# Optimization experiments

Hardware: AMD Instinct MI355X
Metric: run time of the kernel (lower is better)

The kernel has to match this reference:

```python
import jax, jax.numpy as jnp
import numpy as np

N, E, IN, H, C, ED = 100000, 1600000, 128, 4, 32, 16
HC = H * C
NEG_SLOPE = 0.2
EPS = 1e-5


def setup_inputs() -> dict:
    key = jax.random.key(0)
    ks = jax.random.split(key, 12)
    x = jax.random.normal(ks[0], (N, IN), jnp.float32)
    edge_index = jax.random.randint(ks[1], (2, E), 0, N, dtype=jnp.int32)
    edge_attr = jax.random.normal(ks[2], (E, ED), jnp.float32)
    s_in = 1.0 / np.sqrt(IN)
    s_ed = 1.0 / np.sqrt(ED)
    s_c = 1.0 / np.sqrt(C)
    Wl = jax.random.normal(ks[3], (IN, HC), jnp.float32) * s_in
    bl = jnp.zeros((HC,), jnp.float32)
    Wr = jax.random.normal(ks[4], (IN, HC), jnp.float32) * s_in
    br = jnp.zeros((HC,), jnp.float32)
    We = jax.random.normal(ks[5], (ED, HC), jnp.float32) * s_ed
    att = jax.random.normal(ks[6], (H, C), jnp.float32) * s_c
    bias = jnp.zeros((HC,), jnp.float32)
    ln_weight = jnp.ones((HC,), jnp.float32)
    ln_bias = jnp.zeros((HC,), jnp.float32)
    return {"x": x, "edge_index": edge_index, "edge_attr": edge_attr,
            "Wl": Wl, "bl": bl, "Wr": Wr, "br": br, "We": We,
            "att": att, "bias": bias, "ln_weight": ln_weight, "ln_bias": ln_bias}


def gatv2_block(x, src, dst, edge_attr, Wl, bl, Wr, br, We, att, bias, ln_weight, ln_bias):
    n = x.shape[0]
    xl = (x @ Wl + bl).reshape(n, H, C)  # source-side transform
    xr = (x @ Wr + br).reshape(n, H, C)  # target-side transform
    # add_self_loops with fill_value='mean': self-loop edge_attr = mean of
    # incoming edge_attr per node (0 for isolated nodes)
    ea_sum = jax.ops.segment_sum(edge_attr, dst, num_segments=n)
    cnt = jax.ops.segment_sum(jnp.ones((edge_attr.shape[0],), edge_attr.dtype), dst, num_segments=n)
    self_attr = ea_sum / jnp.maximum(cnt, 1.0)[:, None]
    loop = jnp.arange(n, dtype=src.dtype)
    src_a = jnp.concatenate([src, loop])
    dst_a = jnp.concatenate([dst, loop])
    ea_a = jnp.concatenate([edge_attr, self_attr], axis=0)
    e_emb = (ea_a @ We).reshape(-1, H, C)
    # GATv2 attention: a^T LeakyReLU(xl_j + xr_i + e)
    m = xl[src_a] + xr[dst_a] + e_emb            # [Etot, H, C]
    m = jax.nn.leaky_relu(m, NEG_SLOPE)
    alpha = jnp.einsum('ehc,hc->eh', m, att)     # [Etot, H]
    amax = jax.ops.segment_max(alpha, dst_a, num_segments=n)
    alpha = jnp.exp(alpha - amax[dst_a])
    denom = jax.ops.segment_sum(alpha, dst_a, num_segments=n)
    alpha = alpha / denom[dst_a]
    out = jax.ops.segment_sum(xl[src_a] * alpha[:, :, None], dst_a, num_segments=n)
    h = out.reshape(n, HC) + bias
    # residual (in_dim == H*C so no projection), PyG graph-mode LayerNorm
    z = x + h
    mu = jnp.mean(z)
    var = jnp.mean((z - mu) ** 2)
    z = (z - mu) / jnp.sqrt(var + EPS)
    z = z * ln_weight + ln_bias
    return jax.nn.relu(z)  # dropout = identity in eval


def reference(x, edge_index, edge_attr, Wl, bl, Wr, br, We, att, bias, ln_weight, ln_bias):
    src, dst = edge_index[0], edge_index[1]
    return gatv2_block(x, src, dst, edge_attr, Wl, bl, Wr, br, We, att, bias, ln_weight, ln_bias)
```

## Files before the change

kernel.cpp:

```cpp
#include <hip/hip_runtime.h>
#include <hip/hip_bf16.h>

static constexpr float NEG_SLOPE = 0.2f;
static constexpr float LN_EPS = 1e-5f;

typedef float v2f __attribute__((ext_vector_type(2)));
typedef __attribute__((ext_vector_type(8))) short bf16x8;
typedef __attribute__((ext_vector_type(4))) float f32x4;

__device__ __forceinline__ unsigned f2b(float f) {
  unsigned u = __float_as_uint(f);
  return (u + 0x7fffu + ((u >> 16) & 1u)) >> 16;
}
__device__ __forceinline__ v2f b2f2(ushort2 u) {
  v2f r;
  r.x = __uint_as_float((unsigned)u.x << 16);
  r.y = __uint_as_float((unsigned)u.y << 16);
  return r;
}
__device__ __forceinline__ float sbl(unsigned w) {
  return __uint_as_float(w << 16);
}
__device__ __forceinline__ float sbh(unsigned w) {
  return __uint_as_float(w & 0xFFFF0000u);
}

__device__ __forceinline__ float head_sum16(float x) {
  float t;
  t = __int_as_float(__builtin_amdgcn_update_dpp(
      0, __float_as_int(x), 0xB1, 0xF, 0xF, true));
  x += t;
  t = __int_as_float(__builtin_amdgcn_update_dpp(
      0, __float_as_int(x), 0x4E, 0xF, 0xF, true));
  x += t;
  t = __int_as_float(__builtin_amdgcn_update_dpp(
      0, __float_as_int(x), 0x124, 0xF, 0xF, true));
  x += t;
  t = __int_as_float(__builtin_amdgcn_update_dpp(
      0, __float_as_int(x), 0x128, 0xF, 0xF, true));
  x += t;
  return x;
}

__global__ __launch_bounds__(256) void k_packB(
    const float* __restrict__ Wl, const float* __restrict__ Wr,
    const float* __restrict__ bl, const float* __restrict__ br,
    ushort* __restrict__ Bpack, float* __restrict__ bcat,
    int* __restrict__ degcur, int N2, int* __restrict__ tot,
    int* __restrict__ src_pad, double* __restrict__ red)
{
  int tid = blockIdx.x * 256 + threadIdx.x;
  int l = tid & 63, s = (tid >> 6) & 3, t = tid >> 8;
  int col = t * 16 + (l & 15);
  int kb = s * 32 + (l >> 4) * 8;
  const float* __restrict__ W = (col < 128) ? Wl : Wr;
  int c = col & 127;
  unsigned p[4];
#pragma unroll
  for (int i = 0; i < 4; ++i) {
    unsigned lo = f2b(W[(size_t)(kb + 2 * i) * 128 + c]);
    unsigned hi = f2b(W[(size_t)(kb + 2 * i + 1) * 128 + c]);
    p[i] = lo | (hi << 16);
  }
  *(uint4*)(Bpack + (size_t)tid * 8) = make_uint4(p[0], p[1], p[2], p[3]);
  if (tid < 256) bcat[tid] = (tid < 128) ? bl[tid] : br[tid - 128];
  if (tid < 8) src_pad[tid] = 0;
  if (tid < 2) red[tid] = 0.0;
  if (tid == 0) *tot = 0;
  for (int i = tid; i < N2; i += 4096) degcur[i] = 0;
}

__global__ __launch_bounds__(256) void k_gemm_mfma(
    const float* __restrict__ x, const ushort* __restrict__ Bpack,
    const float* __restrict__ bcat, ushort* __restrict__ xl,
    float* __restrict__ outz, int n, const int* __restrict__ dst,
    int* __restrict__ deg, int E)
{
  const int lane = threadIdx.x & 63;
  const int w = threadIdx.x >> 6;
  const int row0 = blockIdx.x * 64 + w * 16;
  const int rowA = min(row0 + (lane & 15), n - 1);
  const int kgrp = lane >> 4;

  f32x4 acc[16];
#pragma unroll
  for (int t = 0; t < 16; ++t) acc[t] = (f32x4){0.f, 0.f, 0.f, 0.f};

#pragma unroll
  for (int s = 0; s < 4; ++s) {
    const float4* ap =
        (const float4*)(x + (size_t)rowA * 128 + s * 32 + kgrp * 8);
    float4 a0 = ap[0], a1 = ap[1];
    bf16x8 a;
    a[0] = (short)f2b(a0.x); a[1] = (short)f2b(a0.y);
    a[2] = (short)f2b(a0.z); a[3] = (short)f2b(a0.w);
    a[4] = (short)f2b(a1.x); a[5] = (short)f2b(a1.y);
    a[6] = (short)f2b(a1.z); a[7] = (short)f2b(a1.w);
#pragma unroll
    for (int t = 0; t < 16; ++t) {
      bf16x8 b =
          *(const bf16x8*)(Bpack + (((size_t)t * 4 + s) * 64 + lane) * 8);
      acc[t] = __builtin_amdgcn_mfma_f32_16x16x32_bf16(a, b, acc[t], 0, 0, 0);
    }
  }

  const int colg = lane & 15;
  const int rbase = row0 + (lane >> 4) * 4;
#pragma unroll
  for (int t = 0; t < 16; ++t) {
    const int col = t * 16 + colg;
    const float bia = bcat[col];
    if (col < 128) {
#pragma unroll
      for (int r = 0; r < 4; ++r) {
        const int R = rbase + r;
        if (R < n) xl[(size_t)R * 128 + col] = (ushort)f2b(acc[t][r] + bia);
      }
    } else {
      const int c = col - 128;
#pragma unroll
      for (int r = 0; r < 4; ++r) {
        const int R = rbase + r;
        if (R < n) outz[(size_t)R * 128 + c] = acc[t][r] + bia;
      }
    }
  }

  for (int e = blockIdx.x * 256 + threadIdx.x; e < E; e += gridDim.x * 256)
    atomicAdd(&deg[dst[e]], 1);
}

__global__ __launch_bounds__(256) void k_allocscan(
    const int* __restrict__ deg, int* __restrict__ offs, int* __restrict__ tot,
    int n)
{
  __shared__ int s[256];
  __shared__ int base;
  const int b = blockIdx.x, t = threadIdx.x, i = b * 256 + t;
  const int v = (i < n) ? deg[i] : 0;
  s[t] = v;
  __syncthreads();
  for (int o = 1; o < 256; o <<= 1) {
    int u = (t >= o) ? s[t - o] : 0;
    __syncthreads();
    s[t] += u;
    __syncthreads();
  }
  if (t == 255) base = atomicAdd(tot, s[255]);
  __syncthreads();
  if (i < n) offs[i] = base + s[t] - v;
}

__global__ __launch_bounds__(256) void k_fill(
    const int* __restrict__ src, const int* __restrict__ dst,
    const int* __restrict__ offs, int* __restrict__ cursor,
    const float4* __restrict__ ea4, int* __restrict__ csr_src,
    ushort* __restrict__ csr_ea, int E)
{
  int e = blockIdx.x * 256 + threadIdx.x;
  if (e >= E) return;
  int d = dst[e];
  int pos = offs[d] + atomicAdd(&cursor[d], 1);
  csr_src[pos] = src[e];
  float4 r0 = ea4[(size_t)e * 4 + 0], r1 = ea4[(size_t)e * 4 + 1];
  float4 r2 = ea4[(size_t)e * 4 + 2], r3 = ea4[(size_t)e * 4 + 3];
  uint4* o4 = (uint4*)(csr_ea + (size_t)pos * 16);
  o4[0] = make_uint4(f2b(r0.x) | (f2b(r0.y) << 16), f2b(r0.z) | (f2b(r0.w) << 16),
                     f2b(r1.x) | (f2b(r1.y) << 16), f2b(r1.z) | (f2b(r1.w) << 16));
  o4[1] = make_uint4(f2b(r2.x) | (f2b(r2.y) << 16), f2b(r2.z) | (f2b(r2.w) << 16),
                     f2b(r3.x) | (f2b(r3.y) << 16), f2b(r3.z) | (f2b(r3.w) << 16));
}

__global__ __launch_bounds__(256) void k_fused(
    const int* __restrict__ csr_src, const ushort* __restrict__ csr_ea,
    const int* __restrict__ offs, const int* __restrict__ deg,
    const ushort* __restrict__ xl, const float* __restrict__ We,
    const float* __restrict__ att, const float* __restrict__ x,
    const float* __restrict__ bias, float* __restrict__ outz,
    double* __restrict__ red, int N)
{
  const int lane = threadIdx.x & 63;
  const int gw =
      __builtin_amdgcn_readfirstlane(blockIdx.x * 4 + (threadIdx.x >> 6));
  const int nw = gridDim.x * 4;
  const v2f* __restrict__ We2 = (const v2f*)We;
  const v2f* __restrict__ X2 = (const v2f*)x;
  v2f* __restrict__ Z2 = (v2f*)outz;

  v2f we[16];
#pragma unroll
  for (int k = 0; k < 16; ++k) we[k] = We2[k * 64 + lane];
  const v2f a2 = ((const v2f*)att)[lane];
  const v2f b2 = ((const v2f*)bias)[lane];

  float sred = 0.f, s2red = 0.f;

  for (int node = gw; node < N; node += nw) {
    const int beg = offs[node];
    const int len = deg[node];
    const v2f xrv = Z2[(size_t)node * 64 + lane];
    const v2f xvSelf =
        b2f2(*(const ushort2*)(xl + (size_t)node * 128 + 2 * lane));

    float dA = 0.f, dB = 0.f;
    v2f aA = {0.f, 0.f}, aB = {0.f, 0.f};
    v2f embsum = {0.f, 0.f};

    auto edgeU = [&](v2f xv, uint4 lo, uint4 hi, float& den, v2f& acc) {
      v2f emb = sbl(lo.x) * we[0];
      emb += sbh(lo.x) * we[1];
      emb += sbl(lo.y) * we[2];
      emb += sbh(lo.y) * we[3];
      emb += sbl(lo.z) * we[4];
      emb += sbh(lo.z) * we[5];
      emb += sbl(lo.w) * we[6];
      emb += sbh(lo.w) * we[7];
      emb += sbl(hi.x) * we[8];
      emb += sbh(hi.x) * we[9];
      emb += sbl(hi.y) * we[10];
      emb += sbh(hi.y) * we[11];
      emb += sbl(hi.z) * we[12];
      emb += sbh(hi.z) * we[13];
      emb += sbl(hi.w) * we[14];
      emb += sbh(hi.w) * we[15];
      embsum += emb;
      v2f mm = xv + xrv + emb;
      v2f ml;
      ml.x = fmaxf(mm.x, NEG_SLOPE * mm.x);
      ml.y = fmaxf(mm.y, NEG_SLOPE * mm.y);
      const float part = head_sum16(fmaf(ml.y, a2.y, ml.x * a2.x));
      const float p = __expf(part);
      den += p;
      acc += xv * p;
    };

    const int nB = len >> 1;
    const int nA = len - nB;
    const int bB = beg + nA;

    uint4 eAlo = {0, 0, 0, 0}, eAhi = {0, 0, 0, 0};
    uint4 eBlo = {0, 0, 0, 0}, eBhi = {0, 0, 0, 0};
    v2f xvA = {0.f, 0.f}, xvB = {0.f, 0.f};
    int sA1 = 0, sB1 = 0;

    if (len > 0) {
      const uint4* pa = (const uint4*)(csr_ea + (size_t)beg * 16);
      eAlo = pa[0];
      eAhi = pa[1];
      const int sA0 = csr_src[beg];
      xvA = b2f2(*(const ushort2*)(xl + (size_t)sA0 * 128 + 2 * lane));
      sA1 = csr_src[beg + 1];
    }
    if (nB > 0) {
      const uint4* pb = (const uint4*)(csr_ea + (size_t)bB * 16);
      eBlo = pb[0];
      eBhi = pb[1];
      const int sB0 = csr_src[bB];
      xvB = b2f2(*(const ushort2*)(xl + (size_t)sB0 * 128 + 2 * lane));
      sB1 = csr_src[bB + 1];
    }

    for (int i = 0; i < nB; ++i) {
      const uint4* pa = (const uint4*)(csr_ea + (size_t)(beg + i + 1) * 16);
      const uint4* pb = (const uint4*)(csr_ea + (size_t)(bB + i + 1) * 16);
      const uint4 nAlo = pa[0], nAhi = pa[1];
      const uint4 nBlo = pb[0], nBhi = pb[1];
      const v2f xvA1 =
          b2f2(*(const ushort2*)(xl + (size_t)sA1 * 128 + 2 * lane));
      const v2f xvB1 =
          b2f2(*(const ushort2*)(xl + (size_t)sB1 * 128 + 2 * lane));
      const int sA2 = csr_src[beg + i + 2];
      const int sB2 = csr_src[bB + i + 2];
      edgeU(xvA, eAlo, eAhi, dA, aA);
      edgeU(xvB, eBlo, eBhi, dB, aB);
      eAlo = nAlo; eAhi = nAhi; eBlo = nBlo; eBhi = nBhi;
      xvA = xvA1; xvB = xvB1;
      sA1 = sA2; sB1 = sB2;
    }
    if (nA > nB) {
      edgeU(xvA, eAlo, eAhi, dA, aA);
    }

    {
      const float inv = (len > 0) ? 1.f / (float)len : 0.f;
      const v2f embS = embsum * inv;
      v2f mm = xvSelf + xrv + embS;
      v2f ml;
      ml.x = fmaxf(mm.x, NEG_SLOPE * mm.x);
      ml.y = fmaxf(mm.y, NEG_SLOPE * mm.y);
      const float part = head_sum16(fmaf(ml.y, a2.y, ml.x * a2.x));
      const float p = __expf(part);
      dA += p;
      aA += xvSelf * p;
    }

    const float den = dA + dB;
    const float invden = 1.f / den;
    const float o0 = (aA.x + aB.x) * invden;
    const float o1 = (aA.y + aB.y) * invden;

    const v2f xvn = X2[(size_t)node * 64 + lane];
    const float v0 = xvn.x + o0 + b2.x;
    const float v1 = xvn.y + o1 + b2.y;
    Z2[(size_t)node * 64 + lane] = (v2f){v0, v1};
    sred += v0 + v1;
    s2red += v0 * v0 + v1 * v1;
  }

#pragma unroll
  for (int o = 32; o > 0; o >>= 1) {
    sred += __shfl_down(sred, o);
    s2red += __shfl_down(s2red, o);
  }
  __shared__ double ls[4], ls2[4];
  const int w = threadIdx.x >> 6;
  if ((threadIdx.x & 63) == 0) {
    ls[w] = (double)sred;
    ls2[w] = (double)s2red;
  }
  __syncthreads();
  if (threadIdx.x == 0) {
    unsafeAtomicAdd(red, ls[0] + ls[1] + ls[2] + ls[3]);
    unsafeAtomicAdd(red + 1, ls2[0] + ls2[1] + ls2[2] + ls2[3]);
  }
}

__global__ __launch_bounds__(256) void k_final(
    float* __restrict__ z, const double* __restrict__ red,
    const float* __restrict__ lnw, const float* __restrict__ lnb, int M4)
{
  int i = blockIdx.x * 256 + threadIdx.x;
  if (i >= M4) return;
  const double invM = 1.0 / ((double)M4 * 4.0);
  const double mu = red[0] * invM;
  const double var = red[1] * invM - mu * mu;
  const float sc = rsqrtf((float)var + LN_EPS);
  const float muf = (float)mu;
  const float4* W4 = (const float4*)lnw;
  const float4* L4 = (const float4*)lnb;
  float4* Z4 = (float4*)z;
  float4 zv = Z4[i], wv = W4[i & 31], lv = L4[i & 31];
  float4 o;
  o.x = fmaxf((zv.x - muf) * sc * wv.x + lv.x, 0.f);
  o.y = fmaxf((zv.y - muf) * sc * wv.y + lv.y, 0.f);
  o.z = fmaxf((zv.z - muf) * sc * wv.z + lv.z, 0.f);
  o.w = fmaxf((zv.w - muf) * sc * wv.w + lv.w, 0.f);
  Z4[i] = o;
}

extern "C" void kernel_launch(void* const* d_in, const int* in_sizes, int n_in,
                              void* d_out, int out_size, void* d_ws,
                              size_t ws_size, hipStream_t stream)
{
  const float* x = (const float*)d_in[0];
  const int* ei = (const int*)d_in[1];
  const float* edge_attr = (const float*)d_in[2];
  const float* Wl = (const float*)d_in[3];
  const float* bl = (const float*)d_in[4];
  const float* Wr = (const float*)d_in[5];
  const float* br = (const float*)d_in[6];
  const float* We = (const float*)d_in[7];
  const float* att = (const float*)d_in[8];
  const float* bias = (const float*)d_in[9];
  const float* lnw = (const float*)d_in[10];
  const float* lnb = (const float*)d_in[11];
  float* out = (float*)d_out;

  const int N = in_sizes[0] / 128;
  const int E = in_sizes[1] / 2;
  const int M = N * 128;
  const int* srcp = ei;
  const int* dstp = ei + E;
  const int nb = (N + 255) / 256;

  ushort* xl = (ushort*)d_ws;
  int* deg = (int*)(xl + (size_t)M);
  int* cursor = deg + N;
  int* offs = cursor + N;
  int* tot = offs + N;
  int* csr_src = tot + 8;
  ushort* csr_ea =
      (ushort*)((((size_t)(csr_src + E + 8)) + 63) & ~(size_t)63);
  double* red = (double*)(
      (((size_t)(csr_ea + (size_t)E * 16 + 64)) + 127) & ~(size_t)127);
  ushort* Bpack = (ushort*)(red + 8);
  float* bcat = (float*)(Bpack + 4096 * 8);

  k_packB<<<16, 256, 0, stream>>>(Wl, Wr, bl, br, Bpack, bcat, deg, 2 * N,
                                  tot, csr_src + E, red);
  k_gemm_mfma<<<(N + 63) / 64, 256, 0, stream>>>(x, Bpack, bcat, xl, out, N,
                                                 dstp, deg, E);
  k_allocscan<<<nb, 256, 0, stream>>>(deg, offs, tot, N);
  k_fill<<<(E + 255) / 256, 256, 0, stream>>>(srcp, dstp, offs, cursor,
                                              (const float4*)edge_attr,
                                              csr_src, csr_ea, E);
  k_fused<<<2048, 256, 0, stream>>>(csr_src, csr_ea, offs, deg, xl, We, att,
                                    x, bias, out, red, N);
  k_final<<<(M / 4 + 255) / 256, 256, 0, stream>>>(out, red, lnw, lnb, M / 4);
}
```

Baseline: 485.2 us.

## Stage edge attributes through double-buffered LDS chunks with cross-node prefetch

Edge attributes for each destination node are now loaded cooperatively in 16-edge chunks (one coalesced 512-byte load across the wave), converted from bf16 to fp32, and written into a per-wave double-buffered LDS slot. The first chunk of the next node is prefetched during the current one. This replaces the old scheme where every lane redundantly loaded the same 32-byte edge record from global memory, with two interleaved edge streams. The price is a single sequential edge stream with less ILP, extra LDS traffic, and a workspace pad enlarged to cover over-reads past the end.

```diff
diff --git a/kernel.cpp b/kernel.cpp
--- a/kernel.cpp
+++ b/kernel.cpp
@@ -180,13 +180,17 @@
     double* __restrict__ red, int N)
 {
   const int lane = threadIdx.x & 63;
-  const int gw =
-      __builtin_amdgcn_readfirstlane(blockIdx.x * 4 + (threadIdx.x >> 6));
+  const int wv = threadIdx.x >> 6;
+  const int gw = __builtin_amdgcn_readfirstlane(blockIdx.x * 4 + wv);
   const int nw = gridDim.x * 4;
+  const uint* __restrict__ eaD = (const uint*)csr_ea;
   const v2f* __restrict__ We2 = (const v2f*)We;
   const v2f* __restrict__ X2 = (const v2f*)x;
   v2f* __restrict__ Z2 = (v2f*)outz;
 
+  __shared__ float sEA[4][2][256];
+  float* const myEA = &sEA[wv][0][0];
+
   v2f we[16];
 #pragma unroll
   for (int k = 0; k < 16; ++k) we[k] = We2[k * 64 + lane];
@@ -195,90 +199,112 @@
 
   float sred = 0.f, s2red = 0.f;
 
-  for (int node = gw; node < N; node += nw) {
-    const int beg = offs[node];
-    const int len = deg[node];
+  int node = gw;
+  int beg = 0, len = 0;
+  if (node < N) {
+    beg = offs[node];
+    len = deg[node];
+  }
+  uint d0 = 0, d1 = 0;
+  if (node < N && len > 0) {
+    const uint* p = eaD + (size_t)beg * 8;
+    d0 = p[lane];
+    d1 = p[lane + 64];
+  }
+
+  while (node < N) {
+    const int nodeN = node + nw;
+    int begN = 0, lenN = 0;
+    if (nodeN < N) {
+      begN = offs[nodeN];
+      lenN = deg[nodeN];
+    }
+
     const v2f xrv = Z2[(size_t)node * 64 + lane];
     const v2f xvSelf =
         b2f2(*(const ushort2*)(xl + (size_t)node * 128 + 2 * lane));
 
-    float dA = 0.f, dB = 0.f;
-    v2f aA = {0.f, 0.f}, aB = {0.f, 0.f};
-    v2f embsum = {0.f, 0.f};
-
-    auto edgeU = [&](v2f xv, uint4 lo, uint4 hi, float& den, v2f& acc) {
-      v2f emb = sbl(lo.x) * we[0];
-      emb += sbh(lo.x) * we[1];
-      emb += sbl(lo.y) * we[2];
-      emb += sbh(lo.y) * we[3];
-      emb += sbl(lo.z) * we[4];
-      emb += sbh(lo.z) * we[5];
-      emb += sbl(lo.w) * we[6];
-      emb += sbh(lo.w) * we[7];
-      emb += sbl(hi.x) * we[8];
-      emb += sbh(hi.x) * we[9];
-      emb += sbl(hi.y) * we[10];
-      emb += sbh(hi.y) * we[11];
-      emb += sbl(hi.z) * we[12];
-      emb += sbh(hi.z) * we[13];
-      emb += sbl(hi.w) * we[14];
-      emb += sbh(hi.w) * we[15];
-      embsum += emb;
-      v2f mm = xv + xrv + emb;
-      v2f ml;
-      ml.x = fmaxf(mm.x, NEG_SLOPE * mm.x);
-      ml.y = fmaxf(mm.y, NEG_SLOPE * mm.y);
-      const float part = head_sum16(fmaf(ml.y, a2.y, ml.x * a2.x));
-      const float p = __expf(part);
-      den += p;
-      acc += xv * p;
-    };
-
-    const int nB = len >> 1;
-    const int nA = len - nB;
-    const int bB = beg + nA;
-
-    uint4 eAlo = {0, 0, 0, 0}, eAhi = {0, 0, 0, 0};
-    uint4 eBlo = {0, 0, 0, 0}, eBhi = {0, 0, 0, 0};
-    v2f xvA = {0.f, 0.f}, xvB = {0.f, 0.f};
-    int sA1 = 0, sB1 = 0;
-
+    float den = 0.f;
+    v2f acc = {0.f, 0.f}, embsum = {0.f, 0.f};
+
+    int buf = 0;
     if (len > 0) {
-      const uint4* pa = (const uint4*)(csr_ea + (size_t)beg * 16);
-      eAlo = pa[0];
-      eAhi = pa[1];
-      const int sA0 = csr_src[beg];
-      xvA = b2f2(*(const ushort2*)(xl + (size_t)sA0 * 128 + 2 * lane));
-      sA1 = csr_src[beg + 1];
-    }
-    if (nB > 0) {
-      const uint4* pb = (const uint4*)(csr_ea + (size_t)bB * 16);
-      eBlo = pb[0];
-      eBhi = pb[1];
-      const int sB0 = csr_src[bB];
-      xvB = b2f2(*(const ushort2*)(xl + (size_t)sB0 * 128 + 2 * lane));
-      sB1 = csr_src[bB + 1];
-    }
-
-    for (int i = 0; i < nB; ++i) {
-      const uint4* pa = (const uint4*)(csr_ea + (size_t)(beg + i + 1) * 16);
-      const uint4* pb = (const uint4*)(csr_ea + (size_t)(bB + i + 1) * 16);
-      const uint4 nAlo = pa[0], nAhi = pa[1];
-      const uint4 nBlo = pb[0], nBhi = pb[1];
-      const v2f xvA1 =
-          b2f2(*(const ushort2*)(xl + (size_t)sA1 * 128 + 2 * lane));
-      const v2f xvB1 =
-          b2f2(*(const ushort2*)(xl + (size_t)sB1 * 128 + 2 * lane));
-      const int sA2 = csr_src[beg + i + 2];
-      const int sB2 = csr_src[bB + i + 2];
-      edgeU(xvA, eAlo, eAhi, dA, aA);
-      edgeU(xvB, eBlo, eBhi, dB, aB);
-      eAlo = nAlo; eAhi = nAhi; eBlo = nBlo; eBhi = nBhi;
-      xvA = xvA1; xvB = xvB1;
-      sA1 = sA2; sB1 = sB2;
-    }
-    if (nA > nB) {
-      edgeU(xvA, eAlo, eAhi, dA, aA);
+      float2* dst = (float2*)myEA;
+      dst[lane] = make_float2(sbl(d0), sbh(d0));
+      dst[lane + 64] = make_float2(sbl(d1), sbh(d1));
+    }
+    const int nchunk = (len + 15) >> 4;
+
+    int g = beg;
+    v2f xvCur = {0.f, 0.f};
+    int sN = 0;
+    if (len > 0) {
+      const int s0 = csr_src[beg];
+      xvCur = b2f2(*(const ushort2*)(xl + (size_t)s0 * 128 + 2 * lane));
+      sN = csr_src[beg + 1];
+    }
+
+    for (int c = 0; c < nchunk; ++c) {
+      if (c + 1 < nchunk) {
+        const uint* p = eaD + (size_t)(beg + (c + 1) * 16) * 8;
+        d0 = p[lane];
+        d1 = p[lane + 64];
+      } else if (nodeN < N && lenN > 0) {
+        const uint* p = eaD + (size_t)begN * 8;
+        d0 = p[lane];
+        d1 = p[lane + 64];
+      }
+      const int m = min(16, len - c * 16);
+      const float* eb = myEA + buf * 256;
+      for (int i = 0; i < m; ++i) {
+        const float4 q0 = *(const float4*)(eb + i * 16);
+        const float4 q1 = *(const float4*)(eb + i * 16 + 4);
+        const float4 q2 = *(const float4*)(eb + i * 16 + 8);
+        const float4 q3 = *(const float4*)(eb + i * 16 + 12);
+        const v2f xvN =
+            b2f2(*(const ushort2*)(xl + (size_t)sN * 128 + 2 * lane));
+        const int sNN = csr_src[g + 2];
+        v2f u0 = q0.x * we[0];
+        v2f u1 = q0.y * we[1];
+        v2f u2 = q0.z * we[2];
+        v2f u3 = q0.w * we[3];
+        u0 += q1.x * we[4];
+        u1 += q1.y * we[5];
+        u2 += q1.z * we[6];
+        u3 += q1.w * we[7];
+        u0 += q2.x * we[8];
+        u1 += q2.y * we[9];
+        u2 += q2.z * we[10];
+        u3 += q2.w * we[11];
+        u0 += q3.x * we[12];
+        u1 += q3.y * we[13];
+        u2 += q3.z * we[14];
+        u3 += q3.w * we[15];
+        const v2f emb = (u0 + u1) + (u2 + u3);
+        embsum += emb;
+        v2f mm = xvCur + xrv + emb;
+        v2f ml;
+        ml.x = fmaxf(mm.x, NEG_SLOPE * mm.x);
+        ml.y = fmaxf(mm.y, NEG_SLOPE * mm.y);
+        const float part = head_sum16(fmaf(ml.y, a2.y, ml.x * a2.x));
+        const float p = __expf(part);
+        den += p;
+        acc += xvCur * p;
+        xvCur = xvN;
+        sN = sNN;
+        ++g;
+      }
+      if (c + 1 < nchunk) {
+        float2* dst = (float2*)(myEA + (buf ^ 1) * 256);
+        dst[lane] = make_float2(sbl(d0), sbh(d0));
+        dst[lane + 64] = make_float2(sbl(d1), sbh(d1));
+        buf ^= 1;
+      }
+    }
+    if (nchunk == 0 && nodeN < N && lenN > 0) {
+      const uint* p = eaD + (size_t)begN * 8;
+      d0 = p[lane];
+      d1 = p[lane + 64];
     }
 
     {
@@ -290,14 +316,13 @@
       ml.y = fmaxf(mm.y, NEG_SLOPE * mm.y);
       const float part = head_sum16(fmaf(ml.y, a2.y, ml.x * a2.x));
       const float p = __expf(part);
-      dA += p;
-      aA += xvSelf * p;
-    }
-
-    const float den = dA + dB;
+      den += p;
+      acc += xvSelf * p;
+    }
+
     const float invden = 1.f / den;
-    const float o0 = (aA.x + aB.x) * invden;
-    const float o1 = (aA.y + aB.y) * invden;
+    const float o0 = acc.x * invden;
+    const float o1 = acc.y * invden;
 
     const v2f xvn = X2[(size_t)node * 64 + lane];
     const float v0 = xvn.x + o0 + b2.x;
@@ -305,6 +330,10 @@
     Z2[(size_t)node * 64 + lane] = (v2f){v0, v1};
     sred += v0 + v1;
     s2red += v0 * v0 + v1 * v1;
+
+    node = nodeN;
+    beg = begN;
+    len = lenN;
   }
 
 #pragma unroll
@@ -313,10 +342,9 @@
     s2red += __shfl_down(s2red, o);
   }
   __shared__ double ls[4], ls2[4];
-  const int w = threadIdx.x >> 6;
   if ((threadIdx.x & 63) == 0) {
-    ls[w] = (double)sred;
-    ls2[w] = (double)s2red;
+    ls[wv] = (double)sred;
+    ls2[wv] = (double)s2red;
   }
   __syncthreads();
   if (threadIdx.x == 0) {
@@ -382,7 +410,7 @@
   ushort* csr_ea =
       (ushort*)((((size_t)(csr_src + E + 8)) + 63) & ~(size_t)63);
   double* red = (double*)(
-      (((size_t)(csr_ea + (size_t)E * 16 + 64)) + 127) & ~(size_t)127);
+      (((size_t)(csr_ea + (size_t)E * 16 + 512)) + 127) & ~(size_t)127);
   ushort* Bpack = (ushort*)(red + 8);
   float* bcat = (float*)(Bpack + 4096 * 8);
 
```

New measurement: 493.3 us. No clear change (+1.7%).

## Pack CSR source index with edge attributes into 64-byte records, deepen prefetch

Applied to the files above, without the earlier changes.

Merges the separate csr_src and csr_ea arrays into a single 64-byte record per edge, holding 16 bf16 attributes plus the source index in an otherwise zero-padded tail. The fused kernel now reads one record per edge and prefetches two edges ahead instead of one, so the source index arrives together with the attributes. This removes a dependent scattered index load, at the cost of doubling the bytes written and read per edge (32 B of padding) and keeping more registers live.

```diff
diff --git a/kernel.cpp b/kernel.cpp
--- a/kernel.cpp
+++ b/kernel.cpp
@@ -47,7 +47,7 @@
     const float* __restrict__ bl, const float* __restrict__ br,
     ushort* __restrict__ Bpack, float* __restrict__ bcat,
     int* __restrict__ degcur, int N2, int* __restrict__ tot,
-    int* __restrict__ src_pad, double* __restrict__ red)
+    uint* __restrict__ rec_pad, double* __restrict__ red)
 {
   int tid = blockIdx.x * 256 + threadIdx.x;
   int l = tid & 63, s = (tid >> 6) & 3, t = tid >> 8;
@@ -64,7 +64,7 @@
   }
   *(uint4*)(Bpack + (size_t)tid * 8) = make_uint4(p[0], p[1], p[2], p[3]);
   if (tid < 256) bcat[tid] = (tid < 128) ? bl[tid] : br[tid - 128];
-  if (tid < 8) src_pad[tid] = 0;
+  if (tid < 32) rec_pad[tid] = 0;
   if (tid < 2) red[tid] = 0.0;
   if (tid == 0) *tot = 0;
   for (int i = tid; i < N2; i += 4096) degcur[i] = 0;
@@ -154,30 +154,29 @@
 __global__ __launch_bounds__(256) void k_fill(
     const int* __restrict__ src, const int* __restrict__ dst,
     const int* __restrict__ offs, int* __restrict__ cursor,
-    const float4* __restrict__ ea4, int* __restrict__ csr_src,
-    ushort* __restrict__ csr_ea, int E)
+    const float4* __restrict__ ea4, uint* __restrict__ rec, int E)
 {
   int e = blockIdx.x * 256 + threadIdx.x;
   if (e >= E) return;
   int d = dst[e];
   int pos = offs[d] + atomicAdd(&cursor[d], 1);
-  csr_src[pos] = src[e];
   float4 r0 = ea4[(size_t)e * 4 + 0], r1 = ea4[(size_t)e * 4 + 1];
   float4 r2 = ea4[(size_t)e * 4 + 2], r3 = ea4[(size_t)e * 4 + 3];
-  uint4* o4 = (uint4*)(csr_ea + (size_t)pos * 16);
+  uint4* o4 = (uint4*)(rec + (size_t)pos * 16);
   o4[0] = make_uint4(f2b(r0.x) | (f2b(r0.y) << 16), f2b(r0.z) | (f2b(r0.w) << 16),
                      f2b(r1.x) | (f2b(r1.y) << 16), f2b(r1.z) | (f2b(r1.w) << 16));
   o4[1] = make_uint4(f2b(r2.x) | (f2b(r2.y) << 16), f2b(r2.z) | (f2b(r2.w) << 16),
                      f2b(r3.x) | (f2b(r3.y) << 16), f2b(r3.z) | (f2b(r3.w) << 16));
+  o4[2] = make_uint4((uint)src[e], 0u, 0u, 0u);
+  o4[3] = make_uint4(0u, 0u, 0u, 0u);
 }
 
 __global__ __launch_bounds__(256) void k_fused(
-    const int* __restrict__ csr_src, const ushort* __restrict__ csr_ea,
-    const int* __restrict__ offs, const int* __restrict__ deg,
-    const ushort* __restrict__ xl, const float* __restrict__ We,
-    const float* __restrict__ att, const float* __restrict__ x,
-    const float* __restrict__ bias, float* __restrict__ outz,
-    double* __restrict__ red, int N)
+    const uint* __restrict__ rec, const int* __restrict__ offs,
+    const int* __restrict__ deg, const ushort* __restrict__ xl,
+    const float* __restrict__ We, const float* __restrict__ att,
+    const float* __restrict__ x, const float* __restrict__ bias,
+    float* __restrict__ outz, double* __restrict__ red, int N)
 {
   const int lane = threadIdx.x & 63;
   const int gw =
@@ -238,47 +237,55 @@
     const int nA = len - nB;
     const int bB = beg + nA;
 
-    uint4 eAlo = {0, 0, 0, 0}, eAhi = {0, 0, 0, 0};
-    uint4 eBlo = {0, 0, 0, 0}, eBhi = {0, 0, 0, 0};
+    uint4 cAlo = {0, 0, 0, 0}, cAhi = {0, 0, 0, 0};
+    uint4 nAlo = {0, 0, 0, 0}, nAhi = {0, 0, 0, 0};
+    uint4 cBlo = {0, 0, 0, 0}, cBhi = {0, 0, 0, 0};
+    uint4 nBlo = {0, 0, 0, 0}, nBhi = {0, 0, 0, 0};
+    int nSrcA = 0, nSrcB = 0;
     v2f xvA = {0.f, 0.f}, xvB = {0.f, 0.f};
-    int sA1 = 0, sB1 = 0;
 
     if (len > 0) {
-      const uint4* pa = (const uint4*)(csr_ea + (size_t)beg * 16);
-      eAlo = pa[0];
-      eAhi = pa[1];
-      const int sA0 = csr_src[beg];
-      xvA = b2f2(*(const ushort2*)(xl + (size_t)sA0 * 128 + 2 * lane));
-      sA1 = csr_src[beg + 1];
+      const uint4* r0 = (const uint4*)(rec + (size_t)beg * 16);
+      cAlo = r0[0];
+      cAhi = r0[1];
+      const int s0 = (int)r0[2].x;
+      xvA = b2f2(*(const ushort2*)(xl + (size_t)s0 * 128 + 2 * lane));
+      const uint4* r1 = (const uint4*)(rec + (size_t)(beg + 1) * 16);
+      nAlo = r1[0];
+      nAhi = r1[1];
+      nSrcA = (int)r1[2].x;
     }
     if (nB > 0) {
-      const uint4* pb = (const uint4*)(csr_ea + (size_t)bB * 16);
-      eBlo = pb[0];
-      eBhi = pb[1];
-      const int sB0 = csr_src[bB];
-      xvB = b2f2(*(const ushort2*)(xl + (size_t)sB0 * 128 + 2 * lane));
-      sB1 = csr_src[bB + 1];
+      const uint4* r0 = (const uint4*)(rec + (size_t)bB * 16);
+      cBlo = r0[0];
+      cBhi = r0[1];
+      const int s0 = (int)r0[2].x;
+      xvB = b2f2(*(const ushort2*)(xl + (size_t)s0 * 128 + 2 * lane));
+      const uint4* r1 = (const uint4*)(rec + (size_t)(bB + 1) * 16);
+      nBlo = r1[0];
+      nBhi = r1[1];
+      nSrcB = (int)r1[2].x;
     }
 
     for (int i = 0; i < nB; ++i) {
-      const uint4* pa = (const uint4*)(csr_ea + (size_t)(beg + i + 1) * 16);
-      const uint4* pb = (const uint4*)(csr_ea + (size_t)(bB + i + 1) * 16);
-      const uint4 nAlo = pa[0], nAhi = pa[1];
-      const uint4 nBlo = pb[0], nBhi = pb[1];
+      const uint4* ra = (const uint4*)(rec + (size_t)(beg + i + 2) * 16);
+      const uint4* rb = (const uint4*)(rec + (size_t)(bB + i + 2) * 16);
+      const uint4 tAlo = ra[0], tAhi = ra[1];
+      const int tSrcA = (int)ra[2].x;
+      const uint4 tBlo = rb[0], tBhi = rb[1];
+      const int tSrcB = (int)rb[2].x;
       const v2f xvA1 =
-          b2f2(*(const ushort2*)(xl + (size_t)sA1 * 128 + 2 * lane));
+          b2f2(*(const ushort2*)(xl + (size_t)nSrcA * 128 + 2 * lane));
       const v2f xvB1 =
-          b2f2(*(const ushort2*)(xl + (size_t)sB1 * 128 + 2 * lane));
-      const int sA2 = csr_src[beg + i + 2];
-      const int sB2 = csr_src[bB + i + 2];
-      edgeU(xvA, eAlo, eAhi, dA, aA);
-      edgeU(xvB, eBlo, eBhi, dB, aB);
-      eAlo = nAlo; eAhi = nAhi; eBlo = nBlo; eBhi = nBhi;
+          b2f2(*(const ushort2*)(xl + (size_t)nSrcB * 128 + 2 * lane));
+      edgeU(xvA, cAlo, cAhi, dA, aA);
+      edgeU(xvB, cBlo, cBhi, dB, aB);
+      cAlo = nAlo; cAhi = nAhi; nAlo = tAlo; nAhi = tAhi; nSrcA = tSrcA;
+      cBlo = nBlo; cBhi = nBhi; nBlo = tBlo; nBhi = tBhi; nSrcB = tSrcB;
       xvA = xvA1; xvB = xvB1;
-      sA1 = sA2; sB1 = sB2;
     }
     if (nA > nB) {
-      edgeU(xvA, eAlo, eAhi, dA, aA);
+      edgeU(xvA, cAlo, cAhi, dA, aA);
     }
 
     {
@@ -378,23 +385,21 @@
   int* cursor = deg + N;
   int* offs = cursor + N;
   int* tot = offs + N;
-  int* csr_src = tot + 8;
-  ushort* csr_ea =
-      (ushort*)((((size_t)(csr_src + E + 8)) + 63) & ~(size_t)63);
+  uint* rec = (uint*)((((size_t)(tot + 8)) + 63) & ~(size_t)63);
   double* red = (double*)(
-      (((size_t)(csr_ea + (size_t)E * 16 + 64)) + 127) & ~(size_t)127);
+      (((size_t)(rec + (size_t)(E + 2) * 16)) + 127) & ~(size_t)127);
   ushort* Bpack = (ushort*)(red + 8);
   float* bcat = (float*)(Bpack + 4096 * 8);
 
   k_packB<<<16, 256, 0, stream>>>(Wl, Wr, bl, br, Bpack, bcat, deg, 2 * N,
-                                  tot, csr_src + E, red);
+                                  tot, rec + (size_t)E * 16, red);
   k_gemm_mfma<<<(N + 63) / 64, 256, 0, stream>>>(x, Bpack, bcat, xl, out, N,
                                                  dstp, deg, E);
   k_allocscan<<<nb, 256, 0, stream>>>(deg, offs, tot, N);
   k_fill<<<(E + 255) / 256, 256, 0, stream>>>(srcp, dstp, offs, cursor,
-                                              (const float4*)edge_attr,
-                                              csr_src, csr_ea, E);
-  k_fused<<<2048, 256, 0, stream>>>(csr_src, csr_ea, offs, deg, xl, We, att,
-                                    x, bias, out, red, N);
+                                              (const float4*)edge_attr, rec,
+                                              E);
+  k_fused<<<2048, 256, 0, stream>>>(rec, offs, deg, xl, We, att, x, bias, out,
+                                    red, N);
   k_final<<<(M / 4 + 255) / 256, 256, 0, stream>>>(out, red, lnw, lnb, M / 4);
 }
```

Result: slower. 513.5 us (+5.8%).
